# Kernel optimization log

Measured on AMD Instinct MI355X. Metric: run time of the kernel, lower is better.

## Reference

```python
import jax, jax.numpy as jnp
import numpy as np

L, E, S, V, B, T = 6, 768, 1024, 32000, 2, 1024
FF = 4 * E
EPS = 1e-5

def _layernorm(v, w, b):
    m = jnp.mean(v, axis=-1, keepdims=True)
    var = jnp.mean((v - m) ** 2, axis=-1, keepdims=True)
    return (v - m) * jax.lax.rsqrt(var + EPS) * w + b

def setup_inputs() -> dict:
    key = jax.random.key(0)
    ks = jax.random.split(key, 12)
    s = 0.02
    n = lambda k, shp: (jax.random.normal(k, shp, jnp.float32) * s)
    return {
        "x": jax.random.randint(ks[0], (B, T), 0, V),
        "tok_emb": n(ks[1], (V, E)),
        "pos_emb": jax.random.normal(ks[2], (S, E), jnp.float32),  # nn.Parameter(randn)
        "Wq": n(ks[3], (L, E, E)), "bq": jnp.zeros((L, E), jnp.float32),
        "Wk": n(ks[4], (L, E, E)), "bk": jnp.zeros((L, E), jnp.float32),
        "Wv": n(ks[5], (L, E, E)), "bv": jnp.zeros((L, E), jnp.float32),
        "ln1w": jnp.ones((L, E), jnp.float32), "ln1b": jnp.zeros((L, E), jnp.float32),
        "W1": n(ks[6], (L, E, FF)), "b1": jnp.zeros((L, FF), jnp.float32),
        "W2": n(ks[7], (L, FF, E)), "b2": jnp.zeros((L, E), jnp.float32),
        "ln2w": jnp.ones((L, E), jnp.float32), "ln2b": jnp.zeros((L, E), jnp.float32),
        "Wo": n(ks[8], (E, V)), "bo": jnp.zeros((V,), jnp.float32),
    }

def reference(x, tok_emb, pos_emb, Wq, bq, Wk, bk, Wv, bv, ln1w, ln1b,
              W1, b1, W2, b2, ln2w, ln2b, Wo, bo):
    t = x.shape[1]
    h = tok_emb[x] + pos_emb[:t]  # [B,T,E]
    scale = jnp.sqrt(jnp.float32(E))
    tril = jnp.tril(jnp.ones((t, t), bool))

    def layer(h, p):
        wq, bq_, wk, bk_, wv, bv_, l1w, l1b, w1, b1_, w2, b2_, l2w, l2b = p
        Q = h @ wq + bq_
        K = h @ wk + bk_
        Vv = h @ wv + bv_
        scores = jnp.einsum('btd,bsd->bts', Q, K) / scale
        # original adds a mask of 1.0 on allowed positions, -inf elsewhere
        masked = jnp.where(tril, scores + 1.0, -jnp.inf)
        A = jax.nn.softmax(masked, axis=-1)
        att = jnp.einsum('bts,bsd->btd', A, Vv)
        h1 = _layernorm(h + att, l1w, l1b)
        ffn = jax.nn.relu(h1 @ w1 + b1_) @ w2 + b2_
        h2 = _layernorm(ffn + h1, l2w, l2b)
        return h2, None

    params = (Wq, bq, Wk, bk, Wv, bv, ln1w, ln1b, W1, b1, W2, b2, ln2w, ln2b)
    h, _ = jax.lax.scan(layer, h, params)
    return h @ Wo + bo  # [B,T,V]
```

## Files before the change

kernel.cpp:

```cpp
#include <hip/hip_runtime.h>
#include <stdint.h>

typedef __bf16 v8bf __attribute__((ext_vector_type(8)));
typedef float  v4f  __attribute__((ext_vector_type(4)));

__device__ __forceinline__ float bf2f(uint16_t h) {
    union { uint32_t u; float f; } x; x.u = ((uint32_t)h) << 16; return x.f;
}
__device__ __forceinline__ uint16_t f2bf(float f) {
    union { float f; uint32_t u; } x; x.f = f;
    uint32_t r = x.u + 0x7fffu + ((x.u >> 16) & 1u);
    return (uint16_t)(r >> 16);
}

__device__ __forceinline__ void gload16(const uint16_t* g, uint16_t* l) {
    __builtin_amdgcn_global_load_lds((const __attribute__((address_space(1))) void*)g,
                                     (__attribute__((address_space(3))) void*)l, 16, 0, 0);
}

__global__ void k_embed(const int* __restrict__ x, const float* __restrict__ tok,
                        const float* __restrict__ pos, float* __restrict__ hf,
                        uint16_t* __restrict__ hb)
{
    int i = blockIdx.x;
    int t = i & 1023;
    int tk = x[i];
    const float* te = tok + (long)tk * 768;
    const float* pe = pos + (long)t * 768;
    for (int j = threadIdx.x; j < 768; j += 256) {
        float v = te[j] + pe[j];
        hf[(long)i * 768 + j] = v;
        hb[(long)i * 768 + j] = f2bf(v);
    }
}

template<typename SrcT>
__global__ void k_transpose(const SrcT* __restrict__ src, uint16_t* __restrict__ dst,
                            int ldS, int ldD, long sBatch, long dBatch)
{
    __shared__ float tile[32][33];
    src += (long)blockIdx.z * sBatch;
    dst += (long)blockIdx.z * dBatch;
    int c0 = blockIdx.x * 32, r0 = blockIdx.y * 32;
    int tx = threadIdx.x, ty = threadIdx.y;
    #pragma unroll
    for (int i = 0; i < 4; ++i) {
        int r = r0 + ty + i * 8;
        SrcT s = src[(long)r * ldS + c0 + tx];
        float v;
        if constexpr (sizeof(SrcT) == 4) v = (float)s; else v = bf2f((uint16_t)s);
        tile[ty + i * 8][tx] = v;
    }
    __syncthreads();
    #pragma unroll
    for (int i = 0; i < 4; ++i) {
        int c = c0 + ty + i * 8;
        dst[(long)c * ldD + r0 + tx] = f2bf(tile[tx][ty + i * 8]);
    }
}

__global__ void k_concat3(const float* __restrict__ a, const float* __restrict__ b,
                          const float* __restrict__ c, float* __restrict__ out)
{
    int l = blockIdx.y;
    const float* s = (blockIdx.x == 0) ? a : ((blockIdx.x == 1) ? b : c);
    s += (long)l * 768;
    for (int j = threadIdx.x; j < 768; j += 256)
        out[(long)l * 2304 + blockIdx.x * 768 + j] = s[j];
}

template<typename OutT, int BN, bool BIAS, bool RELU, bool RES>
__global__ void k_gemmp(const uint16_t* __restrict__ A, const uint16_t* __restrict__ BT,
                        OutT* __restrict__ C, const float* __restrict__ bias,
                        const float* __restrict__ res,
                        int K, int lda, int ldb, int ldc,
                        long bsA, long bsB, long bsC, float scale, int causal)
{
    constexpr int NT = BN / 32;
    constexpr int BOFF = 128 * 32;
    const int nwg = gridDim.x * gridDim.y;
    int lin = blockIdx.y * gridDim.x + blockIdx.x;
    {
        int q = nwg >> 3, r = nwg & 7, x = lin & 7, i = lin >> 3;
        lin = (x < r ? x * (q + 1) : r * (q + 1) + (x - r) * q) + i;
    }
    const int mt = lin % gridDim.y;
    const int nt = lin / gridDim.y;

    if (causal == 1 && nt * BN >= (mt + 1) * 128) return;
    const int Keff = (causal == 2) ? ((mt + 1) * 128 < K ? (mt + 1) * 128 : K) : K;
    const int KT = Keff >> 5;

    __shared__ uint16_t lds[4][(128 + BN) * 32];
    const int tid  = threadIdx.x;
    const int lane = tid & 63;
    const int bz   = blockIdx.z;
    const uint16_t* Ab = A + (long)bz * bsA + (long)mt * 128 * lda;
    const uint16_t* Bb = BT + (long)bz * bsB + (long)nt * BN * ldb;

    const int wm = (tid >> 6) >> 1, wn = (tid >> 6) & 1;
    const int fr = lane & 15, fq = lane >> 4;
    const int swz = (fq ^ (fr & 3)) * 8;

    const int r0  = tid >> 2;
    const int ssl = ((tid & 3) ^ (r0 & 3)) * 8;

    v4f acc[4][NT];
    #pragma unroll
    for (int m = 0; m < 4; ++m)
        #pragma unroll
        for (int n = 0; n < NT; ++n) acc[m][n] = (v4f){0.f, 0.f, 0.f, 0.f};

    #pragma unroll
    for (int t = 0; t < 2; ++t) {
        gload16(Ab + (long)r0 * lda + t * 32 + ssl,        &lds[t][tid * 8]);
        gload16(Ab + (long)(r0 + 64) * lda + t * 32 + ssl, &lds[t][2048 + tid * 8]);
        gload16(Bb + (long)r0 * ldb + t * 32 + ssl,        &lds[t][BOFF + tid * 8]);
        if constexpr (BN == 128)
            gload16(Bb + (long)(r0 + 64) * ldb + t * 32 + ssl, &lds[t][BOFF + 2048 + tid * 8]);
    }

    for (int kti = 0; kti < KT; ++kti) {
        if (kti < KT - 1) {
            if constexpr (BN == 128) asm volatile("s_waitcnt vmcnt(4)" ::: "memory");
            else                     asm volatile("s_waitcnt vmcnt(3)" ::: "memory");
        } else {
            asm volatile("s_waitcnt vmcnt(0)" ::: "memory");
        }
        __builtin_amdgcn_s_barrier();

        const uint16_t* lA = &lds[kti & 3][0];
        const uint16_t* lB = &lds[kti & 3][BOFF];
        v8bf ag[4], bg[NT];
        #pragma unroll
        for (int m = 0; m < 4; ++m)
            ag[m] = *(const v8bf*)&lA[(wm * 64 + m * 16 + fr) * 32 + swz];
        #pragma unroll
        for (int n = 0; n < NT; ++n)
            bg[n] = *(const v8bf*)&lB[(wn * (BN / 2) + n * 16 + fr) * 32 + swz];

        if (kti + 2 < KT) {
            const int ko = (kti + 2) * 32;
            uint16_t* s = &lds[(kti + 2) & 3][0];
            gload16(Ab + (long)r0 * lda + ko + ssl,        &s[tid * 8]);
            gload16(Ab + (long)(r0 + 64) * lda + ko + ssl, &s[2048 + tid * 8]);
            gload16(Bb + (long)r0 * ldb + ko + ssl,        &s[BOFF + tid * 8]);
            if constexpr (BN == 128)
                gload16(Bb + (long)(r0 + 64) * ldb + ko + ssl, &s[BOFF + 2048 + tid * 8]);
        }

        __builtin_amdgcn_s_setprio(1);
        #pragma unroll
        for (int m = 0; m < 4; ++m)
            #pragma unroll
            for (int n = 0; n < NT; ++n)
                acc[m][n] = __builtin_amdgcn_mfma_f32_16x16x32_bf16(ag[m], bg[n], acc[m][n], 0, 0, 0);
        __builtin_amdgcn_s_setprio(0);
    }

    OutT* Cb = C + (long)bz * bsC + (long)mt * 128 * ldc + nt * BN;
    const float* Rb = RES ? (res + (long)bz * bsC + (long)mt * 128 * ldc + nt * BN) : nullptr;
    #pragma unroll
    for (int n = 0; n < NT; ++n) {
        int col = wn * (BN / 2) + n * 16 + fr;
        float bv = BIAS ? bias[nt * BN + col] : 0.f;
        #pragma unroll
        for (int m = 0; m < 4; ++m) {
            #pragma unroll
            for (int r = 0; r < 4; ++r) {
                int row = wm * 64 + m * 16 + fq * 4 + r;
                float v = acc[m][n][r] * scale + bv;
                if (RES) v += Rb[(long)row * ldc + col];
                if (RELU) v = fmaxf(v, 0.f);
                if constexpr (sizeof(OutT) == 4) Cb[(long)row * ldc + col] = v;
                else                             Cb[(long)row * ldc + col] = f2bf(v);
            }
        }
    }
}

__global__ __launch_bounds__(512, 2)
void k_gemm256(const uint16_t* __restrict__ A, const uint16_t* __restrict__ BT,
               float* __restrict__ C, const float* __restrict__ bias,
               int K, int lda, int ldb, int ldc, float scale)
{
    __shared__ uint16_t lds[4][2][8192];

    const int nwg = gridDim.x * gridDim.y;
    int lin = blockIdx.y * gridDim.x + blockIdx.x;
    {
        int q = nwg >> 3, r = nwg & 7, x = lin & 7, i = lin >> 3;
        lin = (x < r ? x * (q + 1) : r * (q + 1) + (x - r) * q) + i;
    }
    const int mt = lin % gridDim.y;
    const int nt = lin / gridDim.y;

    const int tid  = threadIdx.x;
    const int lane = tid & 63;
    const int wid  = tid >> 6;
    const int wm = wid >> 2, wn = wid & 3;
    const int fr = lane & 15, fq = lane >> 4;
    const int swz = (fq ^ (fr & 3)) * 8;

    const uint16_t* Ab = A  + (long)mt * 256 * lda;
    const uint16_t* Bb = BT + (long)nt * 256 * ldb;

    const int srow = tid >> 2;
    const int ssl  = ((tid & 3) ^ (srow & 3)) * 8;
    const int KT   = K >> 5;

    v4f acc[8][4];
    #pragma unroll
    for (int m = 0; m < 8; ++m)
        #pragma unroll
        for (int n = 0; n < 4; ++n) acc[m][n] = (v4f){0.f, 0.f, 0.f, 0.f};

    #pragma unroll
    for (int t = 0; t < 3; ++t) {
        gload16(Ab + (long)srow * lda + t * 32 + ssl,         &lds[t][0][tid * 8]);
        gload16(Ab + (long)(srow + 128) * lda + t * 32 + ssl, &lds[t][0][4096 + tid * 8]);
        gload16(Bb + (long)srow * ldb + t * 32 + ssl,         &lds[t][1][tid * 8]);
        gload16(Bb + (long)(srow + 128) * ldb + t * 32 + ssl, &lds[t][1][4096 + tid * 8]);
    }

    for (int kti = 0; kti < KT; ++kti) {
        if (kti < KT - 2)      asm volatile("s_waitcnt vmcnt(8)" ::: "memory");
        else if (kti == KT - 2) asm volatile("s_waitcnt vmcnt(4)" ::: "memory");
        else                    asm volatile("s_waitcnt vmcnt(0)" ::: "memory");
        __builtin_amdgcn_s_barrier();

        const int ring = kti & 3;
        const uint16_t* lA = &lds[ring][0][0];
        const uint16_t* lB = &lds[ring][1][0];

        v8bf bfr[4], a0[4], a1[4];
        #pragma unroll
        for (int n = 0; n < 4; ++n)
            bfr[n] = *(const v8bf*)&lB[(wn * 64 + n * 16 + fr) * 32 + swz];
        #pragma unroll
        for (int m = 0; m < 4; ++m) {
            a0[m] = *(const v8bf*)&lA[(wm * 128 + m * 16 + fr) * 32 + swz];
            a1[m] = *(const v8bf*)&lA[(wm * 128 + (m + 4) * 16 + fr) * 32 + swz];
        }

        if (kti + 3 < KT) {
            const int ko = (kti + 3) * 32;
            uint16_t* sA = &lds[(kti + 3) & 3][0][0];
            uint16_t* sB = &lds[(kti + 3) & 3][1][0];
            gload16(Ab + (long)srow * lda + ko + ssl,         &sA[tid * 8]);
            gload16(Ab + (long)(srow + 128) * lda + ko + ssl, &sA[4096 + tid * 8]);
            gload16(Bb + (long)srow * ldb + ko + ssl,         &sB[tid * 8]);
            gload16(Bb + (long)(srow + 128) * ldb + ko + ssl, &sB[4096 + tid * 8]);
        }

        __builtin_amdgcn_s_setprio(1);
        #pragma unroll
        for (int m = 0; m < 4; ++m)
            #pragma unroll
            for (int n = 0; n < 4; ++n)
                acc[m][n] = __builtin_amdgcn_mfma_f32_16x16x32_bf16(a0[m], bfr[n], acc[m][n], 0, 0, 0);
        #pragma unroll
        for (int m = 0; m < 4; ++m)
            #pragma unroll
            for (int n = 0; n < 4; ++n)
                acc[m + 4][n] = __builtin_amdgcn_mfma_f32_16x16x32_bf16(a1[m], bfr[n], acc[m + 4][n], 0, 0, 0);
        __builtin_amdgcn_s_setprio(0);
    }

    float* Cb = C + (long)(mt * 256 + wm * 128) * ldc + nt * 256 + wn * 64;
    #pragma unroll
    for (int n = 0; n < 4; ++n) {
        int col = n * 16 + fr;
        float bv = bias[nt * 256 + wn * 64 + col];
        #pragma unroll
        for (int m = 0; m < 8; ++m) {
            #pragma unroll
            for (int r = 0; r < 4; ++r) {
                int row = m * 16 + fq * 4 + r;
                Cb[(long)row * ldc + col] = acc[m][n][r] * scale + bv;
            }
        }
    }
}

__global__ void k_softmax(const float* __restrict__ S, uint16_t* __restrict__ P)
{
    int t = blockIdx.x, b = blockIdx.y;
    const float* row = S + ((long)b * 1024 + t) * 1024;
    uint16_t* pr = P + ((long)b * 1024 + t) * 1024;
    int limit = (t & ~127) + 128;
    int s0 = threadIdx.x * 4;
    float vals[4] = {0.f, 0.f, 0.f, 0.f};
    if (s0 < limit) {
        float4 vv = *(const float4*)(row + s0);
        vals[0] = vv.x; vals[1] = vv.y; vals[2] = vv.z; vals[3] = vv.w;
    }
    float mx = -1e30f;
    #pragma unroll
    for (int j = 0; j < 4; ++j) if (s0 + j <= t) mx = fmaxf(mx, vals[j]);
    #pragma unroll
    for (int o = 32; o; o >>= 1) mx = fmaxf(mx, __shfl_xor(mx, o));
    __shared__ float red[8];
    int wave = threadIdx.x >> 6, lane = threadIdx.x & 63;
    if (lane == 0) red[wave] = mx;
    __syncthreads();
    mx = fmaxf(fmaxf(red[0], red[1]), fmaxf(red[2], red[3]));
    float e[4]; float sum = 0.f;
    #pragma unroll
    for (int j = 0; j < 4; ++j) { e[j] = (s0 + j <= t) ? __expf(vals[j] - mx) : 0.f; sum += e[j]; }
    #pragma unroll
    for (int o = 32; o; o >>= 1) sum += __shfl_xor(sum, o);
    if (lane == 0) red[4 + wave] = sum;
    __syncthreads();
    sum = red[4] + red[5] + red[6] + red[7];
    float inv = 1.f / sum;
    if (s0 < limit) {
        #pragma unroll
        for (int j = 0; j < 4; ++j) pr[s0 + j] = f2bf(e[j] * inv);
    }
}

__global__ void k_ln(const float* __restrict__ a,
                     const float* __restrict__ w, const float* __restrict__ bias,
                     float* __restrict__ outf, uint16_t* __restrict__ outb)
{
    int row = blockIdx.x;
    const float* ar = a + (long)row * 768;
    float v[3]; float s1 = 0.f, s2 = 0.f;
    #pragma unroll
    for (int i = 0; i < 3; ++i) {
        int e = threadIdx.x + i * 256;
        v[i] = ar[e];
        s1 += v[i]; s2 += v[i] * v[i];
    }
    #pragma unroll
    for (int o = 32; o; o >>= 1) { s1 += __shfl_xor(s1, o); s2 += __shfl_xor(s2, o); }
    __shared__ float red[8];
    int wave = threadIdx.x >> 6, lane = threadIdx.x & 63;
    if (lane == 0) { red[wave] = s1; red[4 + wave] = s2; }
    __syncthreads();
    s1 = red[0] + red[1] + red[2] + red[3];
    s2 = red[4] + red[5] + red[6] + red[7];
    float mean = s1 * (1.f / 768.f);
    float var  = s2 * (1.f / 768.f) - mean * mean;
    float rstd = rsqrtf(var + 1e-5f);
    #pragma unroll
    for (int i = 0; i < 3; ++i) {
        int e = threadIdx.x + i * 256;
        float o = (v[i] - mean) * rstd * w[e] + bias[e];
        outf[(long)row * 768 + e] = o;
        outb[(long)row * 768 + e] = f2bf(o);
    }
}

__global__ void k_ln_ffn2(const float* __restrict__ p, long pstride,
                          const float* __restrict__ b2, const float* __restrict__ h1,
                          const float* __restrict__ w, const float* __restrict__ bias,
                          float* __restrict__ outf, uint16_t* __restrict__ outb)
{
    int row = blockIdx.x;
    long base = (long)row * 768;
    float v[3]; float s1 = 0.f, s2 = 0.f;
    #pragma unroll
    for (int i = 0; i < 3; ++i) {
        int e = threadIdx.x + i * 256;
        float acc = b2[e] + h1[base + e];
        #pragma unroll
        for (int s = 0; s < 4; ++s) acc += p[base + e + s * pstride];
        v[i] = acc;
        s1 += acc; s2 += acc * acc;
    }
    #pragma unroll
    for (int o = 32; o; o >>= 1) { s1 += __shfl_xor(s1, o); s2 += __shfl_xor(s2, o); }
    __shared__ float red[8];
    int wave = threadIdx.x >> 6, lane = threadIdx.x & 63;
    if (lane == 0) { red[wave] = s1; red[4 + wave] = s2; }
    __syncthreads();
    s1 = red[0] + red[1] + red[2] + red[3];
    s2 = red[4] + red[5] + red[6] + red[7];
    float mean = s1 * (1.f / 768.f);
    float var  = s2 * (1.f / 768.f) - mean * mean;
    float rstd = rsqrtf(var + 1e-5f);
    #pragma unroll
    for (int i = 0; i < 3; ++i) {
        int e = threadIdx.x + i * 256;
        float o = (v[i] - mean) * rstd * w[e] + bias[e];
        outf[base + e] = o;
        outb[base + e] = f2bf(o);
    }
}

extern "C" void kernel_launch(void* const* d_in, const int* in_sizes, int n_in,
                              void* d_out, int out_size, void* d_ws, size_t ws_size,
                              hipStream_t stream)
{
    const int*   x       = (const int*)d_in[0];
    const float* tok_emb = (const float*)d_in[1];
    const float* pos_emb = (const float*)d_in[2];
    const float* Wq  = (const float*)d_in[3];
    const float* bq  = (const float*)d_in[4];
    const float* Wk  = (const float*)d_in[5];
    const float* bk  = (const float*)d_in[6];
    const float* Wv  = (const float*)d_in[7];
    const float* bv  = (const float*)d_in[8];
    const float* ln1w = (const float*)d_in[9];
    const float* ln1b = (const float*)d_in[10];
    const float* W1  = (const float*)d_in[11];
    const float* b1  = (const float*)d_in[12];
    const float* W2  = (const float*)d_in[13];
    const float* b2  = (const float*)d_in[14];
    const float* ln2w = (const float*)d_in[15];
    const float* ln2b = (const float*)d_in[16];
    const float* Wo  = (const float*)d_in[17];
    const float* bo  = (const float*)d_in[18];
    float* out = (float*)d_out;
    (void)in_sizes; (void)n_in; (void)out_size;

    char* ws = (char*)d_ws;
    size_t off = 0;
    auto alloc = [&](size_t bytes) -> char* {
        char* p = ws + off;
        off = (off + bytes + 255) & ~(size_t)255;
        return p;
    };
    uint16_t* WoT   = (uint16_t*)alloc(32000L * 768 * 2);
    float*    hf    = (float*)alloc(2048L * 768 * 4);
    uint16_t* hb    = (uint16_t*)alloc(2048L * 768 * 2);
    uint16_t* qkv   = (uint16_t*)alloc(2048L * 2304 * 2);
    uint16_t* vT    = (uint16_t*)alloc(2L * 768 * 1024 * 2);
    float*    sc    = (float*)alloc(2L * 1024 * 1024 * 4);
    uint16_t* pr    = (uint16_t*)alloc(2L * 1024 * 1024 * 2);
    float*    hsum  = (float*)alloc(2048L * 768 * 4);
    float*    h1f   = (float*)alloc(2048L * 768 * 4);
    uint16_t* h1b   = (uint16_t*)alloc(2048L * 768 * 2);
    uint16_t* f1    = (uint16_t*)alloc(2048L * 3072 * 2);
    float*    f2p   = (float*)alloc(4L * 2048 * 768 * 4);
    float*    bqkvA = (float*)alloc(6L * 2304 * 4);
    const long PSTR = 2048L * 768;

    size_t mark = off;
    uint16_t* WqkvTA = (uint16_t*)alloc(6L * 2304 * 768 * 2);
    uint16_t* W1TA   = (uint16_t*)alloc(6L * 3072 * 768 * 2);
    uint16_t* W2TA   = (uint16_t*)alloc(6L * 768 * 3072 * 2);
    bool hoist = (off <= ws_size);
    uint16_t *WqkvT = nullptr, *W1T = nullptr, *W2T = nullptr;
    if (!hoist) {
        off = mark;
        WqkvT = (uint16_t*)alloc(2304L * 768 * 2);
        W1T   = (uint16_t*)alloc(3072L * 768 * 2);
        W2T   = (uint16_t*)alloc(768L * 3072 * 2);
    }

    dim3 tb(32, 8);
    const float iscale = 0.036084391824351615f;
    const long EE = 768L * 768;

    k_transpose<float><<<dim3(1000, 24, 1), tb, 0, stream>>>(Wo, WoT, 32000, 768, 0, 0);
    k_embed<<<2048, 256, 0, stream>>>(x, tok_emb, pos_emb, hf, hb);
    k_concat3<<<dim3(3, 6), 256, 0, stream>>>(bq, bk, bv, bqkvA);

    if (hoist) {
        k_transpose<float><<<dim3(24, 24, 6), tb, 0, stream>>>(Wq, WqkvTA,             768, 768, EE, 2304L*768);
        k_transpose<float><<<dim3(24, 24, 6), tb, 0, stream>>>(Wk, WqkvTA + 768L*768,  768, 768, EE, 2304L*768);
        k_transpose<float><<<dim3(24, 24, 6), tb, 0, stream>>>(Wv, WqkvTA + 1536L*768, 768, 768, EE, 2304L*768);
        k_transpose<float><<<dim3(96, 24, 6), tb, 0, stream>>>(W1, W1TA, 3072, 768, 768L*3072, 3072L*768);
        k_transpose<float><<<dim3(24, 96, 6), tb, 0, stream>>>(W2, W2TA, 768, 3072, 3072L*768, 768L*3072);
    }

    for (int l = 0; l < 6; ++l) {
        uint16_t* WqkvL = hoist ? (WqkvTA + l * 2304L * 768) : WqkvT;
        uint16_t* W1L   = hoist ? (W1TA   + l * 3072L * 768) : W1T;
        uint16_t* W2L   = hoist ? (W2TA   + l * 768L * 3072) : W2T;
        if (!hoist) {
            k_transpose<float><<<dim3(24, 24, 1), tb, 0, stream>>>(Wq + l * EE, WqkvT,             768, 768, 0, 0);
            k_transpose<float><<<dim3(24, 24, 1), tb, 0, stream>>>(Wk + l * EE, WqkvT + 768L*768,  768, 768, 0, 0);
            k_transpose<float><<<dim3(24, 24, 1), tb, 0, stream>>>(Wv + l * EE, WqkvT + 1536L*768, 768, 768, 0, 0);
            k_transpose<float><<<dim3(96, 24, 1), tb, 0, stream>>>(W1 + l * 768L * 3072, W1T, 3072, 768, 0, 0);
            k_transpose<float><<<dim3(24, 96, 1), tb, 0, stream>>>(W2 + l * 3072L * 768, W2T, 768, 3072, 0, 0);
        }

        k_gemmp<uint16_t, 64, true, false, false><<<dim3(36, 16, 1), 256, 0, stream>>>(
            hb, WqkvL, qkv, bqkvA + l * 2304, nullptr, 768, 768, 768, 2304, 0, 0, 0, 1.f, 0);
        k_gemmp<float, 64, false, false, false><<<dim3(16, 8, 2), 256, 0, stream>>>(
            qkv, qkv + 768, sc, nullptr, nullptr, 768, 2304, 2304, 1024,
            1024L * 2304, 1024L * 2304, 1024L * 1024, iscale, 1);
        k_softmax<<<dim3(1024, 2), 256, 0, stream>>>(sc, pr);
        k_transpose<uint16_t><<<dim3(24, 32, 2), tb, 0, stream>>>(
            qkv + 1536, vT, 2304, 1024, 1024L * 2304, 768L * 1024);
        k_gemmp<float, 64, false, false, true><<<dim3(12, 8, 2), 256, 0, stream>>>(
            pr, vT, hsum, nullptr, hf, 1024, 1024, 1024, 768,
            1024L * 1024, 768L * 1024, 1024L * 768, 1.f, 2);
        k_ln<<<2048, 256, 0, stream>>>(hsum, ln1w + l * 768, ln1b + l * 768, h1f, h1b);
        k_gemmp<uint16_t, 64, true, true, false><<<dim3(48, 16, 1), 256, 0, stream>>>(
            h1b, W1L, f1, b1 + l * 3072, nullptr, 768, 768, 768, 3072, 0, 0, 0, 1.f, 0);
        k_gemmp<float, 64, false, false, false><<<dim3(12, 16, 4), 256, 0, stream>>>(
            f1, W2L, f2p, nullptr, nullptr, 768, 3072, 3072, 768,
            768, 768, PSTR, 1.f, 0);
        k_ln_ffn2<<<2048, 256, 0, stream>>>(f2p, PSTR, b2 + l * 768, h1f,
                                            ln2w + l * 768, ln2b + l * 768, hf, hb);
    }

    k_gemm256<<<dim3(125, 8, 1), 512, 0, stream>>>(
        hb, WoT, out, bo, 768, 768, 768, 32000, 1.f);
}
```

Before: 884.2 us.

## Shrink output-projection GEMM tile to 256x128 with 3-stage ring and nontemporal stores

The final vocab-projection GEMM drops from 256x256 tiles to 256x128 tiles. The LDS ring shrinks from 4 to 3 stages with prefetch distance 2, and the per-wave accumulators are halved. Launch bounds rise to 4 blocks per CU and the grid doubles to 250x8, aiming for higher occupancy and better wave balance across CUs. Output stores become nontemporal to avoid polluting cache with the large 256MB logits, at the cost of less A-tile reuse per block and a shallower pipeline.

```diff
diff --git a/kernel.cpp b/kernel.cpp
--- a/kernel.cpp
+++ b/kernel.cpp
@@ -179,12 +179,12 @@
     }
 }
 
-__global__ __launch_bounds__(512, 2)
+__global__ __launch_bounds__(512, 4)
 void k_gemm256(const uint16_t* __restrict__ A, const uint16_t* __restrict__ BT,
                float* __restrict__ C, const float* __restrict__ bias,
                int K, int lda, int ldb, int ldc, float scale)
 {
-    __shared__ uint16_t lds[4][2][8192];
+    __shared__ uint16_t lds[3][12288];
 
     const int nwg = gridDim.x * gridDim.y;
     int lin = blockIdx.y * gridDim.x + blockIdx.x;
@@ -198,86 +198,71 @@
     const int tid  = threadIdx.x;
     const int lane = tid & 63;
     const int wid  = tid >> 6;
-    const int wm = wid >> 2, wn = wid & 3;
+    const int wm = wid >> 1, wn = wid & 1;
     const int fr = lane & 15, fq = lane >> 4;
     const int swz = (fq ^ (fr & 3)) * 8;
 
     const uint16_t* Ab = A  + (long)mt * 256 * lda;
-    const uint16_t* Bb = BT + (long)nt * 256 * ldb;
+    const uint16_t* Bb = BT + (long)nt * 128 * ldb;
 
     const int srow = tid >> 2;
     const int ssl  = ((tid & 3) ^ (srow & 3)) * 8;
     const int KT   = K >> 5;
 
-    v4f acc[8][4];
-    #pragma unroll
-    for (int m = 0; m < 8; ++m)
+    v4f acc[4][4];
+    #pragma unroll
+    for (int m = 0; m < 4; ++m)
         #pragma unroll
         for (int n = 0; n < 4; ++n) acc[m][n] = (v4f){0.f, 0.f, 0.f, 0.f};
 
-    #pragma unroll
-    for (int t = 0; t < 3; ++t) {
-        gload16(Ab + (long)srow * lda + t * 32 + ssl,         &lds[t][0][tid * 8]);
-        gload16(Ab + (long)(srow + 128) * lda + t * 32 + ssl, &lds[t][0][4096 + tid * 8]);
-        gload16(Bb + (long)srow * ldb + t * 32 + ssl,         &lds[t][1][tid * 8]);
-        gload16(Bb + (long)(srow + 128) * ldb + t * 32 + ssl, &lds[t][1][4096 + tid * 8]);
-    }
+    auto stage = [&](int t) {
+        const int ko = t * 32;
+        uint16_t* s = &lds[t % 3][0];
+        gload16(Ab + (long)srow * lda + ko + ssl,         &s[tid * 8]);
+        gload16(Ab + (long)(srow + 128) * lda + ko + ssl, &s[4096 + tid * 8]);
+        gload16(Bb + (long)srow * ldb + ko + ssl,         &s[8192 + tid * 8]);
+    };
+
+    for (int t = 0; t < 2 && t < KT; ++t) stage(t);
 
     for (int kti = 0; kti < KT; ++kti) {
-        if (kti < KT - 2)      asm volatile("s_waitcnt vmcnt(8)" ::: "memory");
-        else if (kti == KT - 2) asm volatile("s_waitcnt vmcnt(4)" ::: "memory");
-        else                    asm volatile("s_waitcnt vmcnt(0)" ::: "memory");
+        if (kti < KT - 1) asm volatile("s_waitcnt vmcnt(3)" ::: "memory");
+        else              asm volatile("s_waitcnt vmcnt(0)" ::: "memory");
         __builtin_amdgcn_s_barrier();
 
-        const int ring = kti & 3;
-        const uint16_t* lA = &lds[ring][0][0];
-        const uint16_t* lB = &lds[ring][1][0];
-
-        v8bf bfr[4], a0[4], a1[4];
+        const uint16_t* lA = &lds[kti % 3][0];
+        const uint16_t* lB = &lds[kti % 3][8192];
+
+        v8bf ag[4], bg[4];
+        #pragma unroll
+        for (int m = 0; m < 4; ++m)
+            ag[m] = *(const v8bf*)&lA[(wm * 64 + m * 16 + fr) * 32 + swz];
         #pragma unroll
         for (int n = 0; n < 4; ++n)
-            bfr[n] = *(const v8bf*)&lB[(wn * 64 + n * 16 + fr) * 32 + swz];
-        #pragma unroll
-        for (int m = 0; m < 4; ++m) {
-            a0[m] = *(const v8bf*)&lA[(wm * 128 + m * 16 + fr) * 32 + swz];
-            a1[m] = *(const v8bf*)&lA[(wm * 128 + (m + 4) * 16 + fr) * 32 + swz];
-        }
-
-        if (kti + 3 < KT) {
-            const int ko = (kti + 3) * 32;
-            uint16_t* sA = &lds[(kti + 3) & 3][0][0];
-            uint16_t* sB = &lds[(kti + 3) & 3][1][0];
-            gload16(Ab + (long)srow * lda + ko + ssl,         &sA[tid * 8]);
-            gload16(Ab + (long)(srow + 128) * lda + ko + ssl, &sA[4096 + tid * 8]);
-            gload16(Bb + (long)srow * ldb + ko + ssl,         &sB[tid * 8]);
-            gload16(Bb + (long)(srow + 128) * ldb + ko + ssl, &sB[4096 + tid * 8]);
-        }
+            bg[n] = *(const v8bf*)&lB[(wn * 64 + n * 16 + fr) * 32 + swz];
+
+        if (kti + 2 < KT) stage(kti + 2);
 
         __builtin_amdgcn_s_setprio(1);
         #pragma unroll
         for (int m = 0; m < 4; ++m)
             #pragma unroll
             for (int n = 0; n < 4; ++n)
-                acc[m][n] = __builtin_amdgcn_mfma_f32_16x16x32_bf16(a0[m], bfr[n], acc[m][n], 0, 0, 0);
-        #pragma unroll
-        for (int m = 0; m < 4; ++m)
-            #pragma unroll
-            for (int n = 0; n < 4; ++n)
-                acc[m + 4][n] = __builtin_amdgcn_mfma_f32_16x16x32_bf16(a1[m], bfr[n], acc[m + 4][n], 0, 0, 0);
+                acc[m][n] = __builtin_amdgcn_mfma_f32_16x16x32_bf16(ag[m], bg[n], acc[m][n], 0, 0, 0);
         __builtin_amdgcn_s_setprio(0);
     }
 
-    float* Cb = C + (long)(mt * 256 + wm * 128) * ldc + nt * 256 + wn * 64;
+    float* Cb = C + (long)(mt * 256 + wm * 64) * ldc + nt * 128 + wn * 64;
     #pragma unroll
     for (int n = 0; n < 4; ++n) {
         int col = n * 16 + fr;
-        float bv = bias[nt * 256 + wn * 64 + col];
-        #pragma unroll
-        for (int m = 0; m < 8; ++m) {
+        float bv = bias[nt * 128 + wn * 64 + col];
+        #pragma unroll
+        for (int m = 0; m < 4; ++m) {
             #pragma unroll
             for (int r = 0; r < 4; ++r) {
                 int row = m * 16 + fq * 4 + r;
-                Cb[(long)row * ldc + col] = acc[m][n][r] * scale + bv;
+                __builtin_nontemporal_store(acc[m][n][r] * scale + bv, &Cb[(long)row * ldc + col]);
             }
         }
     }
@@ -500,6 +485,6 @@
                                             ln2w + l * 768, ln2b + l * 768, hf, hb);
     }
 
-    k_gemm256<<<dim3(125, 8, 1), 512, 0, stream>>>(
+    k_gemm256<<<dim3(250, 8, 1), 512, 0, stream>>>(
         hb, WoT, out, bo, 768, 768, 768, 32000, 1.f);
 }
```

Result: no change. 881.4 us (-0.3%).
